# Optimization experiments

Measured on AMD Instinct MI355X. Metric: run time of the kernel, lower is better.

The kernel has to match this reference:

```python
import jax, jax.numpy as jnp
import numpy as np

NUM_GRAPHS = 512
N_NODES = 500000
C = 256
R = 16

def setup_inputs() -> dict:
    key = jax.random.key(0)
    k1, k2, k3, k4 = jax.random.split(key, 4)
    x = jax.random.normal(k1, (N_NODES, C), dtype=jnp.float32)
    batch = jnp.sort(jax.random.randint(k2, (N_NODES,), 0, NUM_GRAPHS, dtype=jnp.int64))
    # Linear weights (torch stores [out,in]; we use [in,out] for x @ W)
    W1 = jax.random.normal(k3, (C, C // R), dtype=jnp.float32) * (1.0 / np.sqrt(C))
    W2 = jax.random.normal(k4, (C // R, C), dtype=jnp.float32) * (1.0 / np.sqrt(C // R))
    return {"x": x, "batch": batch, "W1": W1, "W2": W2}

def reference(x, batch, W1, W2):
    batch = batch.astype(jnp.int32)
    # segment mean pool: [G, C]
    seg_sum = jax.ops.segment_sum(x, batch, num_segments=NUM_GRAPHS)
    counts = jax.ops.segment_sum(jnp.ones((x.shape[0],), x.dtype), batch, num_segments=NUM_GRAPHS)
    mean_pool = seg_sum / jnp.maximum(counts, 1.0)[:, None]
    # squeeze-excite MLP: Linear -> ReLU -> Linear -> Sigmoid
    scale = jax.nn.sigmoid(jax.nn.relu(mean_pool @ W1) @ W2)  # [G, C]
    # repeat_interleave(scale, bincount(batch)) on sorted batch == gather by batch
    return x * scale[batch]
```

## Files before the change

kernel.cpp:

```cpp
#include <hip/hip_runtime.h>

#define NCH 256
#define NGRAPH 512
#define HID 16

typedef __attribute__((ext_vector_type(4))) float f32x4;

__global__ __launch_bounds__(1024, 8) void graph_se_kernel(
    const float* __restrict__ x,
    const int* __restrict__ batch,
    const float* __restrict__ W1,
    const float* __restrict__ W2,
    float* __restrict__ out,
    int n)
{
    const int g   = blockIdx.x;
    const int tid = threadIdx.x;

    __shared__ int   s_se[2];
    __shared__ float s_part[16][NCH];
    __shared__ float s_vec[NCH];
    __shared__ float s_hp[HID][17];
    __shared__ float s_h[HID];

    if (tid < 2) {
        int v = g + tid;
        int lo = 0, hi = n;
        while (lo < hi) { int mid = (lo + hi) >> 1; if (batch[mid] < v) lo = mid + 1; else hi = mid; }
        s_se[tid] = lo;
    }
    __syncthreads();
    const int start = s_se[0], end = s_se[1];
    const int cnt   = end - start;

    const int rg = tid >> 6;
    const int c4 = tid & 63;
    const size_t coff = (size_t)c4 * 4;

    f32x4 acc = (f32x4)(0.f);
    int r = start + rg;
    for (; r + 48 < end; r += 64) {
        f32x4 v0 = *reinterpret_cast<const f32x4*>(x + (size_t)(r     ) * NCH + coff);
        f32x4 v1 = *reinterpret_cast<const f32x4*>(x + (size_t)(r + 16) * NCH + coff);
        f32x4 v2 = *reinterpret_cast<const f32x4*>(x + (size_t)(r + 32) * NCH + coff);
        f32x4 v3 = *reinterpret_cast<const f32x4*>(x + (size_t)(r + 48) * NCH + coff);
        acc += v0 + v1 + v2 + v3;
    }
    for (; r < end; r += 16) {
        acc += *reinterpret_cast<const f32x4*>(x + (size_t)r * NCH + coff);
    }
    *reinterpret_cast<f32x4*>(&s_part[rg][c4 * 4]) = acc;
    __syncthreads();

    if (tid < NCH) {
        float m = 0.f;
        #pragma unroll
        for (int i = 0; i < 16; ++i) m += s_part[i][tid];
        m *= (cnt > 0) ? (1.0f / (float)cnt) : 1.0f;
        s_vec[tid] = m;
    }
    __syncthreads();

    if (tid < NCH) {
        const int j   = tid >> 4;
        const int sub = tid & 15;
        float hp = 0.f;
        #pragma unroll
        for (int i = 0; i < 16; ++i) {
            int c = sub * 16 + i;
            hp += s_vec[c] * W1[c * HID + j];
        }
        s_hp[j][sub] = hp;
    }
    __syncthreads();
    if (tid < HID) {
        float h = 0.f;
        #pragma unroll
        for (int i = 0; i < 16; ++i) h += s_hp[tid][i];
        s_h[tid] = fmaxf(h, 0.f);
    }
    __syncthreads();

    if (tid < NCH) {
        float sc = 0.f;
        #pragma unroll
        for (int j = 0; j < HID; ++j) sc += s_h[j] * W2[j * NCH + tid];
        s_vec[tid] = 1.0f / (1.0f + __expf(-sc));
    }
    __syncthreads();

    const f32x4 scv = *reinterpret_cast<const f32x4*>(&s_vec[c4 * 4]);
    r = start + rg;
    for (; r + 16 < end; r += 32) {
        f32x4 v0 = *reinterpret_cast<const f32x4*>(x + (size_t)(r     ) * NCH + coff);
        f32x4 v1 = *reinterpret_cast<const f32x4*>(x + (size_t)(r + 16) * NCH + coff);
        f32x4 o0 = v0 * scv;
        f32x4 o1 = v1 * scv;
        __builtin_nontemporal_store(o0, reinterpret_cast<f32x4*>(out + (size_t)(r     ) * NCH + coff));
        __builtin_nontemporal_store(o1, reinterpret_cast<f32x4*>(out + (size_t)(r + 16) * NCH + coff));
    }
    if (r < end) {
        f32x4 v0 = *reinterpret_cast<const f32x4*>(x + (size_t)r * NCH + coff);
        f32x4 o0 = v0 * scv;
        __builtin_nontemporal_store(o0, reinterpret_cast<f32x4*>(out + (size_t)r * NCH + coff));
    }
}

extern "C" void kernel_launch(void* const* d_in, const int* in_sizes, int n_in,
                              void* d_out, int out_size, void* d_ws, size_t ws_size,
                              hipStream_t stream) {
    const float* x     = (const float*)d_in[0];
    const int*   batch = (const int*)d_in[1];
    const float* W1    = (const float*)d_in[2];
    const float* W2    = (const float*)d_in[3];
    float*       out   = (float*)d_out;
    const int n = in_sizes[1];

    hipLaunchKernelGGL(graph_se_kernel, dim3(NGRAPH), dim3(1024), 0, stream,
                       x, batch, W1, W2, out, n);
}
```

Baseline: 293.8 us.

## Process two graphs per block, overlapping graph A scaling with graph B pooling

Each of 256 blocks now handles graphs b and b+256. After graph A's pool and MLP, half the warps write A's scaled output while the other half compute graph B's segment sum, then B's MLP and output follow. The aim is to hide the serial MLP phase and barrier stalls behind memory streaming, and to cut the block count to one wave of 256 CUs. In exchange, each phase of a graph runs on half the threads, load balance depends on segment sizes, and the loads are unrolled deeper.

```diff
diff --git a/kernel.cpp b/kernel.cpp
--- a/kernel.cpp
+++ b/kernel.cpp
@@ -1,75 +1,35 @@
 #include <hip/hip_runtime.h>
 
 #define NCH 256
-#define NGRAPH 512
 #define HID 16
+#define NBLK 256
 
 typedef __attribute__((ext_vector_type(4))) float f32x4;
 
-__global__ __launch_bounds__(1024, 8) void graph_se_kernel(
-    const float* __restrict__ x,
-    const int* __restrict__ batch,
-    const float* __restrict__ W1,
-    const float* __restrict__ W2,
-    float* __restrict__ out,
-    int n)
+__device__ __forceinline__ f32x4 ldrow(const float* __restrict__ x, int r, size_t coff) {
+    return *reinterpret_cast<const f32x4*>(x + (size_t)r * NCH + coff);
+}
+
+__device__ __forceinline__ void se_mlp(const float* __restrict__ W1,
+                                       const float* __restrict__ W2,
+                                       float (&s_part)[16][NCH],
+                                       int first, int npart, int cnt,
+                                       float* __restrict__ s_vec,
+                                       float (&s_hp)[HID][17], float (&s_h)[HID],
+                                       int tid)
 {
-    const int g   = blockIdx.x;
-    const int tid = threadIdx.x;
-
-    __shared__ int   s_se[2];
-    __shared__ float s_part[16][NCH];
-    __shared__ float s_vec[NCH];
-    __shared__ float s_hp[HID][17];
-    __shared__ float s_h[HID];
-
-    if (tid < 2) {
-        int v = g + tid;
-        int lo = 0, hi = n;
-        while (lo < hi) { int mid = (lo + hi) >> 1; if (batch[mid] < v) lo = mid + 1; else hi = mid; }
-        s_se[tid] = lo;
-    }
-    __syncthreads();
-    const int start = s_se[0], end = s_se[1];
-    const int cnt   = end - start;
-
-    const int rg = tid >> 6;
-    const int c4 = tid & 63;
-    const size_t coff = (size_t)c4 * 4;
-
-    f32x4 acc = (f32x4)(0.f);
-    int r = start + rg;
-    for (; r + 48 < end; r += 64) {
-        f32x4 v0 = *reinterpret_cast<const f32x4*>(x + (size_t)(r     ) * NCH + coff);
-        f32x4 v1 = *reinterpret_cast<const f32x4*>(x + (size_t)(r + 16) * NCH + coff);
-        f32x4 v2 = *reinterpret_cast<const f32x4*>(x + (size_t)(r + 32) * NCH + coff);
-        f32x4 v3 = *reinterpret_cast<const f32x4*>(x + (size_t)(r + 48) * NCH + coff);
-        acc += v0 + v1 + v2 + v3;
-    }
-    for (; r < end; r += 16) {
-        acc += *reinterpret_cast<const f32x4*>(x + (size_t)r * NCH + coff);
-    }
-    *reinterpret_cast<f32x4*>(&s_part[rg][c4 * 4]) = acc;
-    __syncthreads();
-
     if (tid < NCH) {
         float m = 0.f;
-        #pragma unroll
-        for (int i = 0; i < 16; ++i) m += s_part[i][tid];
+        for (int i = 0; i < npart; ++i) m += s_part[first + i][tid];
         m *= (cnt > 0) ? (1.0f / (float)cnt) : 1.0f;
         s_vec[tid] = m;
     }
     __syncthreads();
-
     if (tid < NCH) {
-        const int j   = tid >> 4;
-        const int sub = tid & 15;
+        const int j = tid >> 4, sub = tid & 15;
         float hp = 0.f;
         #pragma unroll
-        for (int i = 0; i < 16; ++i) {
-            int c = sub * 16 + i;
-            hp += s_vec[c] * W1[c * HID + j];
-        }
+        for (int i = 0; i < 16; ++i) { int c = sub * 16 + i; hp += s_vec[c] * W1[c * HID + j]; }
         s_hp[j][sub] = hp;
     }
     __syncthreads();
@@ -80,29 +40,129 @@
         s_h[tid] = fmaxf(h, 0.f);
     }
     __syncthreads();
-
     if (tid < NCH) {
         float sc = 0.f;
         #pragma unroll
         for (int j = 0; j < HID; ++j) sc += s_h[j] * W2[j * NCH + tid];
         s_vec[tid] = 1.0f / (1.0f + __expf(-sc));
     }
+}
+
+__global__ __launch_bounds__(1024, 4) void graph_se_kernel(
+    const float* __restrict__ x,
+    const int* __restrict__ batch,
+    const float* __restrict__ W1,
+    const float* __restrict__ W2,
+    float* __restrict__ out,
+    int n)
+{
+    const int b   = blockIdx.x;
+    const int tid = threadIdx.x;
+
+    __shared__ int   s_bnd[4];
+    __shared__ float s_part[16][NCH];
+    __shared__ float s_vecA[NCH];
+    __shared__ float s_vecB[NCH];
+    __shared__ float s_hp[HID][17];
+    __shared__ float s_h[HID];
+
+    if (tid < 4) {
+        int v = (tid < 2) ? (b + tid) : (NBLK + b + (tid - 2));
+        int lo = 0, hi = n;
+        while (lo < hi) { int mid = (lo + hi) >> 1; if (batch[mid] < v) lo = mid + 1; else hi = mid; }
+        s_bnd[tid] = lo;
+    }
+    __syncthreads();
+    const int loA = s_bnd[0], hiA = s_bnd[1];
+    const int loB = s_bnd[2], hiB = s_bnd[3];
+
+    const int rg = tid >> 6;
+    const int c4 = tid & 63;
+    const size_t coff = (size_t)c4 * 4;
+
+    {
+        f32x4 acc = (f32x4)(0.f);
+        int r = loA + rg;
+        for (; r + 112 < hiA; r += 128) {
+            f32x4 v0 = ldrow(x, r      , coff);
+            f32x4 v1 = ldrow(x, r +  16, coff);
+            f32x4 v2 = ldrow(x, r +  32, coff);
+            f32x4 v3 = ldrow(x, r +  48, coff);
+            f32x4 v4 = ldrow(x, r +  64, coff);
+            f32x4 v5 = ldrow(x, r +  80, coff);
+            f32x4 v6 = ldrow(x, r +  96, coff);
+            f32x4 v7 = ldrow(x, r + 112, coff);
+            acc += ((v0 + v1) + (v2 + v3)) + ((v4 + v5) + (v6 + v7));
+        }
+        for (; r < hiA; r += 16) acc += ldrow(x, r, coff);
+        *reinterpret_cast<f32x4*>(&s_part[rg][c4 * 4]) = acc;
+    }
     __syncthreads();
 
-    const f32x4 scv = *reinterpret_cast<const f32x4*>(&s_vec[c4 * 4]);
-    r = start + rg;
-    for (; r + 16 < end; r += 32) {
-        f32x4 v0 = *reinterpret_cast<const f32x4*>(x + (size_t)(r     ) * NCH + coff);
-        f32x4 v1 = *reinterpret_cast<const f32x4*>(x + (size_t)(r + 16) * NCH + coff);
-        f32x4 o0 = v0 * scv;
-        f32x4 o1 = v1 * scv;
-        __builtin_nontemporal_store(o0, reinterpret_cast<f32x4*>(out + (size_t)(r     ) * NCH + coff));
-        __builtin_nontemporal_store(o1, reinterpret_cast<f32x4*>(out + (size_t)(r + 16) * NCH + coff));
+    se_mlp(W1, W2, s_part, 0, 16, hiA - loA, s_vecA, s_hp, s_h, tid);
+    __syncthreads();
+
+    if (rg < 8) {
+        const f32x4 scv = *reinterpret_cast<const f32x4*>(&s_vecA[c4 * 4]);
+        int r = loA + rg;
+        for (; r + 24 < hiA; r += 32) {
+            f32x4 v0 = ldrow(x, r     , coff);
+            f32x4 v1 = ldrow(x, r +  8, coff);
+            f32x4 v2 = ldrow(x, r + 16, coff);
+            f32x4 v3 = ldrow(x, r + 24, coff);
+            f32x4 o0 = v0 * scv, o1 = v1 * scv, o2 = v2 * scv, o3 = v3 * scv;
+            __builtin_nontemporal_store(o0, reinterpret_cast<f32x4*>(out + (size_t)(r     ) * NCH + coff));
+            __builtin_nontemporal_store(o1, reinterpret_cast<f32x4*>(out + (size_t)(r +  8) * NCH + coff));
+            __builtin_nontemporal_store(o2, reinterpret_cast<f32x4*>(out + (size_t)(r + 16) * NCH + coff));
+            __builtin_nontemporal_store(o3, reinterpret_cast<f32x4*>(out + (size_t)(r + 24) * NCH + coff));
+        }
+        for (; r < hiA; r += 8) {
+            f32x4 v0 = ldrow(x, r, coff);
+            f32x4 o0 = v0 * scv;
+            __builtin_nontemporal_store(o0, reinterpret_cast<f32x4*>(out + (size_t)r * NCH + coff));
+        }
+    } else {
+        const int gid = rg - 8;
+        f32x4 acc = (f32x4)(0.f);
+        int r = loB + gid;
+        for (; r + 56 < hiB; r += 64) {
+            f32x4 v0 = ldrow(x, r     , coff);
+            f32x4 v1 = ldrow(x, r +  8, coff);
+            f32x4 v2 = ldrow(x, r + 16, coff);
+            f32x4 v3 = ldrow(x, r + 24, coff);
+            f32x4 v4 = ldrow(x, r + 32, coff);
+            f32x4 v5 = ldrow(x, r + 40, coff);
+            f32x4 v6 = ldrow(x, r + 48, coff);
+            f32x4 v7 = ldrow(x, r + 56, coff);
+            acc += ((v0 + v1) + (v2 + v3)) + ((v4 + v5) + (v6 + v7));
+        }
+        for (; r < hiB; r += 8) acc += ldrow(x, r, coff);
+        *reinterpret_cast<f32x4*>(&s_part[rg][c4 * 4]) = acc;
     }
-    if (r < end) {
-        f32x4 v0 = *reinterpret_cast<const f32x4*>(x + (size_t)r * NCH + coff);
-        f32x4 o0 = v0 * scv;
-        __builtin_nontemporal_store(o0, reinterpret_cast<f32x4*>(out + (size_t)r * NCH + coff));
+    __syncthreads();
+
+    se_mlp(W1, W2, s_part, 8, 8, hiB - loB, s_vecB, s_hp, s_h, tid);
+    __syncthreads();
+
+    {
+        const f32x4 scv = *reinterpret_cast<const f32x4*>(&s_vecB[c4 * 4]);
+        int r = loB + rg;
+        for (; r + 48 < hiB; r += 64) {
+            f32x4 v0 = ldrow(x, r     , coff);
+            f32x4 v1 = ldrow(x, r + 16, coff);
+            f32x4 v2 = ldrow(x, r + 32, coff);
+            f32x4 v3 = ldrow(x, r + 48, coff);
+            f32x4 o0 = v0 * scv, o1 = v1 * scv, o2 = v2 * scv, o3 = v3 * scv;
+            __builtin_nontemporal_store(o0, reinterpret_cast<f32x4*>(out + (size_t)(r     ) * NCH + coff));
+            __builtin_nontemporal_store(o1, reinterpret_cast<f32x4*>(out + (size_t)(r + 16) * NCH + coff));
+            __builtin_nontemporal_store(o2, reinterpret_cast<f32x4*>(out + (size_t)(r + 32) * NCH + coff));
+            __builtin_nontemporal_store(o3, reinterpret_cast<f32x4*>(out + (size_t)(r + 48) * NCH + coff));
+        }
+        for (; r < hiB; r += 16) {
+            f32x4 v0 = ldrow(x, r, coff);
+            f32x4 o0 = v0 * scv;
+            __builtin_nontemporal_store(o0, reinterpret_cast<f32x4*>(out + (size_t)r * NCH + coff));
+        }
     }
 }
 
@@ -116,6 +176,6 @@
     float*       out   = (float*)d_out;
     const int n = in_sizes[1];
 
-    hipLaunchKernelGGL(graph_se_kernel, dim3(NGRAPH), dim3(1024), 0, stream,
+    hipLaunchKernelGGL(graph_se_kernel, dim3(NBLK), dim3(1024), 0, stream,
                        x, batch, W1, W2, out, n);
 }
```

Result: faster. 266.5 us (-9.3%).

## Split kernel into pooling producer blocks and flag-synchronized writer consumer blocks

Applied to the files above, without the earlier changes.

Replaces the one-block-per-graph design with 64 producer blocks that pool and run the SE MLP for 8 graphs each, and 448 consumer blocks that scale contiguous row chunks. Consumers spin on per-graph flags in workspace memory, so writing can start while later graphs are still being pooled. The aim is to fix load imbalance from uneven graph sizes and overlap the two passes over x. The risk is deadlock if consumer blocks become resident before the producers, plus the cost of spin-waiting and an extra memset launch.

```diff
diff --git a/kernel.cpp b/kernel.cpp
--- a/kernel.cpp
+++ b/kernel.cpp
@@ -3,106 +3,140 @@
 #define NCH 256
 #define NGRAPH 512
 #define HID 16
+#define POOLB 64
+#define WRITEB 448
+#define GPP (NGRAPH / POOLB)
 
 typedef __attribute__((ext_vector_type(4))) float f32x4;
 
-__global__ __launch_bounds__(1024, 8) void graph_se_kernel(
+__device__ __forceinline__ f32x4 ldrow(const float* __restrict__ x, int r, size_t coff) {
+    return *reinterpret_cast<const f32x4*>(x + (size_t)r * NCH + coff);
+}
+
+__device__ __forceinline__ int lower_bound(const int* __restrict__ batch, int n, int v) {
+    int lo = 0, hi = n;
+    while (lo < hi) { int mid = (lo + hi) >> 1; if (batch[mid] < v) lo = mid + 1; else hi = mid; }
+    return lo;
+}
+
+__global__ __launch_bounds__(512, 4) void graph_se_pc(
     const float* __restrict__ x,
     const int* __restrict__ batch,
     const float* __restrict__ W1,
     const float* __restrict__ W2,
     float* __restrict__ out,
+    int* __restrict__ flags,
+    float* __restrict__ scales,
     int n)
 {
-    const int g   = blockIdx.x;
     const int tid = threadIdx.x;
-
-    __shared__ int   s_se[2];
-    __shared__ float s_part[16][NCH];
-    __shared__ float s_vec[NCH];
-    __shared__ float s_hp[HID][17];
-    __shared__ float s_h[HID];
-
-    if (tid < 2) {
-        int v = g + tid;
-        int lo = 0, hi = n;
-        while (lo < hi) { int mid = (lo + hi) >> 1; if (batch[mid] < v) lo = mid + 1; else hi = mid; }
-        s_se[tid] = lo;
-    }
-    __syncthreads();
-    const int start = s_se[0], end = s_se[1];
-    const int cnt   = end - start;
-
-    const int rg = tid >> 6;
-    const int c4 = tid & 63;
+    const int rg  = tid >> 6;
+    const int c4  = tid & 63;
     const size_t coff = (size_t)c4 * 4;
 
-    f32x4 acc = (f32x4)(0.f);
-    int r = start + rg;
-    for (; r + 48 < end; r += 64) {
-        f32x4 v0 = *reinterpret_cast<const f32x4*>(x + (size_t)(r     ) * NCH + coff);
-        f32x4 v1 = *reinterpret_cast<const f32x4*>(x + (size_t)(r + 16) * NCH + coff);
-        f32x4 v2 = *reinterpret_cast<const f32x4*>(x + (size_t)(r + 32) * NCH + coff);
-        f32x4 v3 = *reinterpret_cast<const f32x4*>(x + (size_t)(r + 48) * NCH + coff);
-        acc += v0 + v1 + v2 + v3;
-    }
-    for (; r < end; r += 16) {
-        acc += *reinterpret_cast<const f32x4*>(x + (size_t)r * NCH + coff);
-    }
-    *reinterpret_cast<f32x4*>(&s_part[rg][c4 * 4]) = acc;
-    __syncthreads();
+    if (blockIdx.x < POOLB) {
+        const int p = blockIdx.x;
+        __shared__ float s_part[8][NCH];
+        __shared__ float s_vec[NCH];
+        __shared__ float s_hp[HID][17];
+        __shared__ float s_h[HID];
 
-    if (tid < NCH) {
-        float m = 0.f;
-        #pragma unroll
-        for (int i = 0; i < 16; ++i) m += s_part[i][tid];
-        m *= (cnt > 0) ? (1.0f / (float)cnt) : 1.0f;
-        s_vec[tid] = m;
-    }
-    __syncthreads();
+        for (int k = 0; k < GPP; ++k) {
+            const int g  = k * POOLB + p;
+            const int lo = lower_bound(batch, n, g);
+            const int hi = lower_bound(batch, n, g + 1);
+            const int cnt = hi - lo;
 
-    if (tid < NCH) {
-        const int j   = tid >> 4;
-        const int sub = tid & 15;
-        float hp = 0.f;
-        #pragma unroll
-        for (int i = 0; i < 16; ++i) {
-            int c = sub * 16 + i;
-            hp += s_vec[c] * W1[c * HID + j];
+            f32x4 acc = (f32x4)(0.f);
+            int r = lo + rg;
+            for (; r + 120 < hi; r += 128) {
+                f32x4 t[16];
+                #pragma unroll
+                for (int q = 0; q < 16; ++q) t[q] = ldrow(x, r + 8 * q, coff);
+                #pragma unroll
+                for (int q = 0; q < 16; ++q) acc += t[q];
+            }
+            for (; r < hi; r += 8) acc += ldrow(x, r, coff);
+            *reinterpret_cast<f32x4*>(&s_part[rg][c4 * 4]) = acc;
+            __syncthreads();
+
+            if (tid < NCH) {
+                float m = 0.f;
+                #pragma unroll
+                for (int i = 0; i < 8; ++i) m += s_part[i][tid];
+                m *= (cnt > 0) ? (1.0f / (float)cnt) : 1.0f;
+                s_vec[tid] = m;
+            }
+            __syncthreads();
+            if (tid < NCH) {
+                const int j = tid >> 4, sub = tid & 15;
+                float hp = 0.f;
+                #pragma unroll
+                for (int i = 0; i < 16; ++i) { int c = sub * 16 + i; hp += s_vec[c] * W1[c * HID + j]; }
+                s_hp[j][sub] = hp;
+            }
+            __syncthreads();
+            if (tid < HID) {
+                float h = 0.f;
+                #pragma unroll
+                for (int i = 0; i < 16; ++i) h += s_hp[tid][i];
+                s_h[tid] = fmaxf(h, 0.f);
+            }
+            __syncthreads();
+            if (tid < NCH) {
+                float sc = 0.f;
+                #pragma unroll
+                for (int j = 0; j < HID; ++j) sc += s_h[j] * W2[j * NCH + tid];
+                sc = 1.0f / (1.0f + __expf(-sc));
+                scales[(size_t)g * NCH + tid] = sc;
+                __threadfence();
+            }
+            __syncthreads();
+            if (tid == 0) {
+                __hip_atomic_store(&flags[g], 1, __ATOMIC_RELEASE, __HIP_MEMORY_SCOPE_AGENT);
+            }
+            __syncthreads();
         }
-        s_hp[j][sub] = hp;
-    }
-    __syncthreads();
-    if (tid < HID) {
-        float h = 0.f;
-        #pragma unroll
-        for (int i = 0; i < 16; ++i) h += s_hp[tid][i];
-        s_h[tid] = fmaxf(h, 0.f);
-    }
-    __syncthreads();
+    } else {
+        const int w = blockIdx.x - POOLB;
+        const int chunk = (n + WRITEB - 1) / WRITEB;
+        const int r0 = w * chunk;
+        const int r1 = min(n, r0 + chunk);
 
-    if (tid < NCH) {
-        float sc = 0.f;
-        #pragma unroll
-        for (int j = 0; j < HID; ++j) sc += s_h[j] * W2[j * NCH + tid];
-        s_vec[tid] = 1.0f / (1.0f + __expf(-sc));
-    }
-    __syncthreads();
+        int rs = r0;
+        while (rs < r1) {
+            const int g = batch[rs];
+            int lo2 = rs + 1, hi2 = r1;
+            while (lo2 < hi2) { int mid = (lo2 + hi2) >> 1; if (batch[mid] <= g) lo2 = mid + 1; else hi2 = mid; }
+            const int re = lo2;
 
-    const f32x4 scv = *reinterpret_cast<const f32x4*>(&s_vec[c4 * 4]);
-    r = start + rg;
-    for (; r + 16 < end; r += 32) {
-        f32x4 v0 = *reinterpret_cast<const f32x4*>(x + (size_t)(r     ) * NCH + coff);
-        f32x4 v1 = *reinterpret_cast<const f32x4*>(x + (size_t)(r + 16) * NCH + coff);
-        f32x4 o0 = v0 * scv;
-        f32x4 o1 = v1 * scv;
-        __builtin_nontemporal_store(o0, reinterpret_cast<f32x4*>(out + (size_t)(r     ) * NCH + coff));
-        __builtin_nontemporal_store(o1, reinterpret_cast<f32x4*>(out + (size_t)(r + 16) * NCH + coff));
-    }
-    if (r < end) {
-        f32x4 v0 = *reinterpret_cast<const f32x4*>(x + (size_t)r * NCH + coff);
-        f32x4 o0 = v0 * scv;
-        __builtin_nontemporal_store(o0, reinterpret_cast<f32x4*>(out + (size_t)r * NCH + coff));
+            if (tid == 0) {
+                while (__hip_atomic_load(&flags[g], __ATOMIC_ACQUIRE, __HIP_MEMORY_SCOPE_AGENT) == 0)
+                    __builtin_amdgcn_s_sleep(32);
+            }
+            __syncthreads();
+
+            const f32x4 scv = *reinterpret_cast<const f32x4*>(scales + (size_t)g * NCH + coff);
+
+            int r = rs + rg;
+            for (; r + 24 < re; r += 32) {
+                f32x4 v0 = ldrow(x, r     , coff);
+                f32x4 v1 = ldrow(x, r +  8, coff);
+                f32x4 v2 = ldrow(x, r + 16, coff);
+                f32x4 v3 = ldrow(x, r + 24, coff);
+                f32x4 o0 = v0 * scv, o1 = v1 * scv, o2 = v2 * scv, o3 = v3 * scv;
+                __builtin_nontemporal_store(o0, reinterpret_cast<f32x4*>(out + (size_t)(r     ) * NCH + coff));
+                __builtin_nontemporal_store(o1, reinterpret_cast<f32x4*>(out + (size_t)(r +  8) * NCH + coff));
+                __builtin_nontemporal_store(o2, reinterpret_cast<f32x4*>(out + (size_t)(r + 16) * NCH + coff));
+                __builtin_nontemporal_store(o3, reinterpret_cast<f32x4*>(out + (size_t)(r + 24) * NCH + coff));
+            }
+            for (; r < re; r += 8) {
+                f32x4 v0 = ldrow(x, r, coff);
+                f32x4 o0 = v0 * scv;
+                __builtin_nontemporal_store(o0, reinterpret_cast<f32x4*>(out + (size_t)r * NCH + coff));
+            }
+            rs = re;
+        }
     }
 }
 
@@ -116,6 +150,10 @@
     float*       out   = (float*)d_out;
     const int n = in_sizes[1];
 
-    hipLaunchKernelGGL(graph_se_kernel, dim3(NGRAPH), dim3(1024), 0, stream,
-                       x, batch, W1, W2, out, n);
+    int*   flags  = (int*)d_ws;
+    float* scales = (float*)((char*)d_ws + 4096);
+
+    hipMemsetAsync(flags, 0, NGRAPH * sizeof(int), stream);
+    hipLaunchKernelGGL(graph_se_pc, dim3(POOLB + WRITEB), dim3(512), 0, stream,
+                       x, batch, W1, W2, out, flags, scales, n);
 }
```

After: 1.119 ms. 3.81x slower.

## Split fused per-graph kernel into pool+MLP kernel and grid-stride scale kernel

Applied to the files above, without the earlier changes.

Replaces the single per-graph kernel with two launches. The first pools each graph with 512 threads and 8 rows in flight per thread, runs the MLP, and writes per-graph scales to workspace. The second is a flat grid-stride elementwise kernel that multiplies x by the scale gathered through batch, which balances work across the GPU regardless of graph size. The cost is a second launch, an extra gather of batch and scales per vector, and dropping the nontemporal stores.

```diff
diff --git a/kernel.cpp b/kernel.cpp
--- a/kernel.cpp
+++ b/kernel.cpp
@@ -6,19 +6,23 @@
 
 typedef __attribute__((ext_vector_type(4))) float f32x4;
 
-__global__ __launch_bounds__(1024, 8) void graph_se_kernel(
+__device__ __forceinline__ f32x4 ldrow(const float* __restrict__ x, int r, size_t coff) {
+    return *reinterpret_cast<const f32x4*>(x + (size_t)r * NCH + coff);
+}
+
+__global__ __launch_bounds__(512, 4) void pool_mlp_kernel(
     const float* __restrict__ x,
     const int* __restrict__ batch,
     const float* __restrict__ W1,
     const float* __restrict__ W2,
-    float* __restrict__ out,
+    float* __restrict__ scales,
     int n)
 {
     const int g   = blockIdx.x;
     const int tid = threadIdx.x;
 
     __shared__ int   s_se[2];
-    __shared__ float s_part[16][NCH];
+    __shared__ float s_part[8][NCH];
     __shared__ float s_vec[NCH];
     __shared__ float s_hp[HID][17];
     __shared__ float s_h[HID];
@@ -39,37 +43,34 @@
 
     f32x4 acc = (f32x4)(0.f);
     int r = start + rg;
-    for (; r + 48 < end; r += 64) {
-        f32x4 v0 = *reinterpret_cast<const f32x4*>(x + (size_t)(r     ) * NCH + coff);
-        f32x4 v1 = *reinterpret_cast<const f32x4*>(x + (size_t)(r + 16) * NCH + coff);
-        f32x4 v2 = *reinterpret_cast<const f32x4*>(x + (size_t)(r + 32) * NCH + coff);
-        f32x4 v3 = *reinterpret_cast<const f32x4*>(x + (size_t)(r + 48) * NCH + coff);
-        acc += v0 + v1 + v2 + v3;
+    for (; r + 56 < end; r += 64) {
+        f32x4 v0 = ldrow(x, r     , coff);
+        f32x4 v1 = ldrow(x, r +  8, coff);
+        f32x4 v2 = ldrow(x, r + 16, coff);
+        f32x4 v3 = ldrow(x, r + 24, coff);
+        f32x4 v4 = ldrow(x, r + 32, coff);
+        f32x4 v5 = ldrow(x, r + 40, coff);
+        f32x4 v6 = ldrow(x, r + 48, coff);
+        f32x4 v7 = ldrow(x, r + 56, coff);
+        acc += ((v0 + v1) + (v2 + v3)) + ((v4 + v5) + (v6 + v7));
     }
-    for (; r < end; r += 16) {
-        acc += *reinterpret_cast<const f32x4*>(x + (size_t)r * NCH + coff);
-    }
+    for (; r < end; r += 8) acc += ldrow(x, r, coff);
     *reinterpret_cast<f32x4*>(&s_part[rg][c4 * 4]) = acc;
     __syncthreads();
 
     if (tid < NCH) {
         float m = 0.f;
         #pragma unroll
-        for (int i = 0; i < 16; ++i) m += s_part[i][tid];
+        for (int i = 0; i < 8; ++i) m += s_part[i][tid];
         m *= (cnt > 0) ? (1.0f / (float)cnt) : 1.0f;
         s_vec[tid] = m;
     }
     __syncthreads();
-
     if (tid < NCH) {
-        const int j   = tid >> 4;
-        const int sub = tid & 15;
+        const int j = tid >> 4, sub = tid & 15;
         float hp = 0.f;
         #pragma unroll
-        for (int i = 0; i < 16; ++i) {
-            int c = sub * 16 + i;
-            hp += s_vec[c] * W1[c * HID + j];
-        }
+        for (int i = 0; i < 16; ++i) { int c = sub * 16 + i; hp += s_vec[c] * W1[c * HID + j]; }
         s_hp[j][sub] = hp;
     }
     __syncthreads();
@@ -80,29 +81,45 @@
         s_h[tid] = fmaxf(h, 0.f);
     }
     __syncthreads();
-
     if (tid < NCH) {
         float sc = 0.f;
         #pragma unroll
         for (int j = 0; j < HID; ++j) sc += s_h[j] * W2[j * NCH + tid];
-        s_vec[tid] = 1.0f / (1.0f + __expf(-sc));
+        scales[(size_t)g * NCH + tid] = 1.0f / (1.0f + __expf(-sc));
     }
-    __syncthreads();
+}
 
-    const f32x4 scv = *reinterpret_cast<const f32x4*>(&s_vec[c4 * 4]);
-    r = start + rg;
-    for (; r + 16 < end; r += 32) {
-        f32x4 v0 = *reinterpret_cast<const f32x4*>(x + (size_t)(r     ) * NCH + coff);
-        f32x4 v1 = *reinterpret_cast<const f32x4*>(x + (size_t)(r + 16) * NCH + coff);
-        f32x4 o0 = v0 * scv;
-        f32x4 o1 = v1 * scv;
-        __builtin_nontemporal_store(o0, reinterpret_cast<f32x4*>(out + (size_t)(r     ) * NCH + coff));
-        __builtin_nontemporal_store(o1, reinterpret_cast<f32x4*>(out + (size_t)(r + 16) * NCH + coff));
+__global__ __launch_bounds__(256, 8) void scale_mul_kernel(
+    const float* __restrict__ x,
+    const int* __restrict__ batch,
+    const float* __restrict__ scales,
+    float* __restrict__ out,
+    long long n4)
+{
+    const long long T = (long long)gridDim.x * blockDim.x;
+    long long q0 = (long long)blockIdx.x * blockDim.x + threadIdx.x;
+
+    const f32x4* __restrict__ xv = (const f32x4*)x;
+    f32x4* __restrict__ ov       = (f32x4*)out;
+
+    for (; q0 + 3 * T < n4; q0 += 4 * T) {
+        long long q1 = q0 + T, q2 = q0 + 2 * T, q3 = q0 + 3 * T;
+        f32x4 v0 = xv[q0], v1 = xv[q1], v2 = xv[q2], v3 = xv[q3];
+        int g0 = batch[q0 >> 6], g1 = batch[q1 >> 6], g2 = batch[q2 >> 6], g3 = batch[q3 >> 6];
+        f32x4 s0 = *reinterpret_cast<const f32x4*>(scales + (size_t)g0 * NCH + ((int)q0 & 63) * 4);
+        f32x4 s1 = *reinterpret_cast<const f32x4*>(scales + (size_t)g1 * NCH + ((int)q1 & 63) * 4);
+        f32x4 s2 = *reinterpret_cast<const f32x4*>(scales + (size_t)g2 * NCH + ((int)q2 & 63) * 4);
+        f32x4 s3 = *reinterpret_cast<const f32x4*>(scales + (size_t)g3 * NCH + ((int)q3 & 63) * 4);
+        ov[q0] = v0 * s0;
+        ov[q1] = v1 * s1;
+        ov[q2] = v2 * s2;
+        ov[q3] = v3 * s3;
     }
-    if (r < end) {
-        f32x4 v0 = *reinterpret_cast<const f32x4*>(x + (size_t)r * NCH + coff);
-        f32x4 o0 = v0 * scv;
-        __builtin_nontemporal_store(o0, reinterpret_cast<f32x4*>(out + (size_t)r * NCH + coff));
+    for (; q0 < n4; q0 += T) {
+        f32x4 v = xv[q0];
+        int g = batch[q0 >> 6];
+        f32x4 s = *reinterpret_cast<const f32x4*>(scales + (size_t)g * NCH + ((int)q0 & 63) * 4);
+        ov[q0] = v * s;
     }
 }
 
@@ -116,6 +133,12 @@
     float*       out   = (float*)d_out;
     const int n = in_sizes[1];
 
-    hipLaunchKernelGGL(graph_se_kernel, dim3(NGRAPH), dim3(1024), 0, stream,
-                       x, batch, W1, W2, out, n);
+    float* scales = (float*)d_ws;
+
+    hipLaunchKernelGGL(pool_mlp_kernel, dim3(NGRAPH), dim3(512), 0, stream,
+                       x, batch, W1, W2, scales, n);
+
+    const long long n4 = (long long)n * (NCH / 4);
+    hipLaunchKernelGGL(scale_mul_kernel, dim3(2048), dim3(256), 0, stream,
+                       x, batch, scales, out, n4);
 }
```

After: 338.8 us. 1.15x slower.
